# Optimization experiments

Hardware: AMD Instinct MI355X
Metric: run time of the kernel (lower is better)

## Reference

```python
import jax, jax.numpy as jnp
import numpy as np

NNZ = 4_194_304
IN_FEATURES = 4096
OUT_FEATURES = 4096
BATCH = 4
SEQ = 2048


def setup_inputs() -> dict:
    key = jax.random.key(0)
    k1, k2, k3, k4, k5, k6 = jax.random.split(key, 6)
    x = jax.random.normal(k1, (BATCH, SEQ, IN_FEATURES), dtype=jnp.float32)
    rows = jax.random.randint(k2, (NNZ,), 0, OUT_FEATURES, dtype=jnp.int32)
    cols = jax.random.randint(k3, (NNZ,), 0, IN_FEATURES, dtype=jnp.int32)
    w_real = jax.random.normal(k4, (NNZ,), dtype=jnp.float32)
    w_imag = jax.random.normal(k5, (NNZ,), dtype=jnp.float32)
    phase_angles = jax.random.uniform(k6, (BATCH,), dtype=jnp.float32) * 2.0 * np.pi
    return {
        "x": x,
        "rows": rows,
        "cols": cols,
        "w_real": w_real,
        "w_imag": w_imag,
        "phase_angles": phase_angles,
        "out_features": OUT_FEATURES,
    }


def reference(x, rows, cols, w_real, w_imag, phase_angles, out_features):
    B, S, F_in = x.shape
    N = B * S
    x_flat = x.reshape(N, F_in)  # [N, F_in]
    # per-flattened-row cosine phase (phase is per-batch, repeated over seq)
    cos_p = jnp.cos(jnp.repeat(phase_angles, S))  # [N]
    # assemble sparse COO weights into dense (out, in) matrices (duplicates sum)
    Wr = jnp.zeros((out_features, F_in), dtype=x_flat.dtype).at[rows, cols].add(w_real)
    Wi = jnp.zeros((out_features, F_in), dtype=x_flat.dtype).at[rows, cols].add(w_imag)
    # out[n, r] = sum_e x[n, cols[e]] * (w_real[e] + cos(phase[n]) * w_imag[e])
    out = x_flat @ Wr.T + cos_p[:, None] * (x_flat @ Wi.T)  # [N, out]
    return out.reshape(B, S, out_features)
```

## Files before the change

### kernel.cpp

```cpp
#include <hip/hip_runtime.h>


#define K_IN   4096
#define F_OUT  4096
#define SEQ    2048
#define NROW   8192
#define NNZ    4194304
#define WELEM  16777216
#define NBUCK  1024
#define SEGB   5120

typedef float  f32x4  __attribute__((ext_vector_type(4)));
typedef __bf16 bf16x8 __attribute__((ext_vector_type(8)));
typedef unsigned short u16x8 __attribute__((ext_vector_type(8)));

__device__ __forceinline__ unsigned short f2bf(float f) {
  unsigned u = __builtin_bit_cast(unsigned, f);
  u += 0x7fffu + ((u >> 16) & 1u);
  return (unsigned short)(u >> 16);
}
__device__ __forceinline__ float bf2f(unsigned short b) {
  return __builtin_bit_cast(float, (unsigned)b << 16);
}

__global__ __launch_bounds__(1024) void bin_kernel(
    const int* __restrict__ rows, const int* __restrict__ cols,
    const float* __restrict__ wre, const float* __restrict__ wim,
    unsigned* __restrict__ cursor, unsigned long long* __restrict__ records,
    const float* __restrict__ x, unsigned short* __restrict__ Xb) {
  const int b = blockIdx.x;
  if (b < 256) {
    __shared__ unsigned cnt[NBUCK];
    const int tid = threadIdx.x;
    const int e0 = b << 14;
    cnt[tid] = 0u;
    __syncthreads();
    #pragma unroll
    for (int i = 0; i < 16; ++i)
      atomicAdd(&cnt[((unsigned)rows[e0 + (i << 10) + tid]) >> 2], 1u);
    __syncthreads();
    {
      const unsigned c = cnt[tid];
      unsigned base = 0u;
      if (c) base = atomicAdd(&cursor[tid], c);
      cnt[tid] = base;
    }
    __syncthreads();
    for (int i = 0; i < 16; ++i) {
      const int e = e0 + (i << 10) + tid;
      const unsigned r  = (unsigned)rows[e];
      const unsigned bk = r >> 2;
      const unsigned rank = atomicAdd(&cnt[bk], 1u);
      const unsigned pk = (unsigned)f2bf(wre[e]) | ((unsigned)f2bf(wim[e]) << 16);
      if (rank < SEGB)
        records[(size_t)bk * SEGB + rank] =
            ((unsigned long long)pk << 32) | ((r & 3u) << 12) | (unsigned)cols[e];
    }
  } else {
    const size_t i8 = (((size_t)(b - 256) << 10) + threadIdx.x) << 3;
    f32x4 a = *(const f32x4*)(x + i8);
    f32x4 c = *(const f32x4*)(x + i8 + 4);
    u16x8 v;
    v[0] = f2bf(a[0]); v[1] = f2bf(a[1]); v[2] = f2bf(a[2]); v[3] = f2bf(a[3]);
    v[4] = f2bf(c[0]); v[5] = f2bf(c[1]); v[6] = f2bf(c[2]); v[7] = f2bf(c[3]);
    *(u16x8*)(Xb + i8) = v;
  }
}

__global__ __launch_bounds__(512) void assemble_kernel(
    const unsigned* __restrict__ cursor,
    const unsigned long long* __restrict__ records,
    const float* __restrict__ phase, unsigned short* __restrict__ Wb) {
  __shared__ float accRe[16384];
  __shared__ float accIm[16384];
  const int bk  = blockIdx.x;
  const int tid = threadIdx.x;
  #pragma unroll
  for (int i = 0; i < 32; ++i) {
    accRe[(i << 9) + tid] = 0.f;
    accIm[(i << 9) + tid] = 0.f;
  }
  __syncthreads();
  unsigned cnt = cursor[bk];
  if (cnt > SEGB) cnt = SEGB;
  const unsigned long long* seg = records + (size_t)bk * SEGB;
  for (unsigned i = tid; i < cnt; i += 512) {
    const unsigned long long rec = seg[i];
    const unsigned s = (unsigned)rec & 16383u;
    atomicAdd(&accRe[s], bf2f((unsigned short)((rec >> 32) & 0xffffu)));
    atomicAdd(&accIm[s], bf2f((unsigned short)(rec >> 48)));
  }
  __syncthreads();
  float cb[4];
  cb[0] = cosf(phase[0]); cb[1] = cosf(phase[1]);
  cb[2] = cosf(phase[2]); cb[3] = cosf(phase[3]);
  #pragma unroll
  for (int it = 0; it < 32; ++it) {
    const int s = (it << 9) + tid;
    const float re = accRe[s];
    const float im = accIm[s];
    #pragma unroll
    for (int bb = 0; bb < 4; ++bb)
      Wb[((size_t)bb << 24) + ((size_t)bk << 14) + s] = f2bf(re + cb[bb] * im);
  }
}

#define GLOAD_LDS(g, l)                                                        \
  __builtin_amdgcn_global_load_lds(                                            \
      (const __attribute__((address_space(1))) unsigned int*)(g),              \
      (__attribute__((address_space(3))) unsigned int*)(l), 16, 0, 0)

__global__ __launch_bounds__(512, 2) void gemm_kernel(
    const unsigned short* __restrict__ Xb,
    const unsigned short* __restrict__ Wb,
    float* __restrict__ out) {
  __shared__ unsigned short lds[65536];

  const int tid  = threadIdx.x;
  const int wid  = tid >> 6;
  const int lane = tid & 63;
  const int wr   = wid >> 2;
  const int wc   = wid & 3;

  const int bid  = blockIdx.x;
  const int swz  = ((bid & 7) << 6) | (bid >> 3);
  const int brow = swz >> 4;
  const int bcol = swz & 15;
  const size_t M0 = (size_t)brow << 8;
  const int batch = brow >> 3;
  const unsigned short* Ap = Xb + M0 * K_IN;
  const unsigned short* Bp = Wb + ((size_t)batch << 24) + (((size_t)bcol << 8) * K_IN);

  const int srow = lane >> 3;
  const int gsl  = ((lane & 7) ^ srow) << 3;
  const int lrow = lane & 15;
  const int lr7  = lane & 7;
  const int sb   = lane >> 4;

  f32x4 acc[8][4] = {};

#define STAGE(buf, k0)                                                         \
  {                                                                            \
    _Pragma("unroll")                                                          \
    for (int l = 0; l < 4; ++l) {                                              \
      const int rr = (l << 6) + (wid << 3);                                    \
      GLOAD_LDS(Ap + (size_t)(rr + srow) * K_IN + (size_t)((k0) + gsl),        \
                &lds[((buf) << 15) + (rr << 6)]);                              \
    }                                                                          \
    _Pragma("unroll")                                                          \
    for (int l = 0; l < 4; ++l) {                                              \
      const int rr = (l << 6) + (wid << 3);                                    \
      GLOAD_LDS(Bp + (size_t)(rr + srow) * K_IN + (size_t)((k0) + gsl),        \
                &lds[((buf) << 15) + 16384 + (rr << 6)]);                      \
    }                                                                          \
  }

#define COMPUTE(buf)                                                           \
  {                                                                            \
    const unsigned short* la = &lds[(buf) << 15];                              \
    const unsigned short* lb = &lds[((buf) << 15) + 16384];                    \
    _Pragma("unroll")                                                          \
    for (int t = 0; t < 2; ++t) {                                              \
      const int cs = (((t << 2) + sb) ^ lr7) << 3;                             \
      bf16x8 af[8], bff[4];                                                    \
      _Pragma("unroll")                                                        \
      for (int m = 0; m < 8; ++m)                                              \
        af[m] = *(const bf16x8*)&la[(((wr << 7) + (m << 4) + lrow) << 6) + cs];\
      _Pragma("unroll")                                                        \
      for (int n = 0; n < 4; ++n)                                              \
        bff[n] = *(const bf16x8*)&lb[(((wc << 6) + (n << 4) + lrow) << 6) + cs];\
      __builtin_amdgcn_s_setprio(1);                                           \
      _Pragma("unroll")                                                        \
      for (int m = 0; m < 8; ++m)                                              \
        _Pragma("unroll")                                                      \
        for (int n = 0; n < 4; ++n)                                            \
          acc[m][n] = __builtin_amdgcn_mfma_f32_16x16x32_bf16(                 \
              af[m], bff[n], acc[m][n], 0, 0, 0);                              \
      __builtin_amdgcn_s_setprio(0);                                           \
    }                                                                          \
  }

  STAGE(0, 0);
  int cur = 0;
  for (int t = 0; t < 63; ++t) {
    STAGE(cur ^ 1, (t + 1) << 6);
    asm volatile("s_waitcnt vmcnt(8)\n\ts_barrier" ::: "memory");
    COMPUTE(cur);
    asm volatile("s_barrier" ::: "memory");
    cur ^= 1;
  }
  asm volatile("s_waitcnt vmcnt(0)\n\ts_barrier" ::: "memory");
  COMPUTE(cur);

  const int ch = lane >> 4;
  float* op = out + (M0 + (size_t)(wr << 7)) * F_OUT + ((size_t)bcol << 8) + (wc << 6);
  #pragma unroll
  for (int m = 0; m < 8; ++m)
    #pragma unroll
    for (int n = 0; n < 4; ++n)
      #pragma unroll
      for (int j = 0; j < 4; ++j)
        op[(size_t)((m << 4) + (ch << 2) + j) * F_OUT + (n << 4) + lrow] = acc[m][n][j];
#undef STAGE
#undef COMPUTE
}

__global__ __launch_bounds__(256) void scatter_kernel(
    const int* __restrict__ rows, const int* __restrict__ cols,
    const float* __restrict__ wre, const float* __restrict__ wim,
    unsigned short* __restrict__ Wcb) {
  int e = blockIdx.x * 256 + threadIdx.x;
  int r = rows[e];
  int c = cols[e];
  unsigned pk = (unsigned)f2bf(wre[e]) | ((unsigned)f2bf(wim[e]) << 16);
  size_t idx = ((size_t)r << 12) + (size_t)c;
  asm volatile("global_atomic_pk_add_bf16 %0, %1, off"
               :: "v"(Wcb + (idx << 1)), "v"(pk) : "memory");
}
__global__ __launch_bounds__(256) void fold_kernel(
    const unsigned short* __restrict__ Wcb, const float* __restrict__ phase,
    unsigned short* __restrict__ Wb) {
  size_t i8 = ((size_t)blockIdx.x * 256 + threadIdx.x) << 3;
  float cb[4];
  cb[0] = cosf(phase[0]); cb[1] = cosf(phase[1]);
  cb[2] = cosf(phase[2]); cb[3] = cosf(phase[3]);
  const unsigned short* p = Wcb + (i8 << 1);
  u16x8 a = *(const u16x8*)(p);
  u16x8 b = *(const u16x8*)(p + 8);
  float rr[8], ii[8];
  rr[0] = bf2f(a[0]); ii[0] = bf2f(a[1]);
  rr[1] = bf2f(a[2]); ii[1] = bf2f(a[3]);
  rr[2] = bf2f(a[4]); ii[2] = bf2f(a[5]);
  rr[3] = bf2f(a[6]); ii[3] = bf2f(a[7]);
  rr[4] = bf2f(b[0]); ii[4] = bf2f(b[1]);
  rr[5] = bf2f(b[2]); ii[5] = bf2f(b[3]);
  rr[6] = bf2f(b[4]); ii[6] = bf2f(b[5]);
  rr[7] = bf2f(b[6]); ii[7] = bf2f(b[7]);
  #pragma unroll
  for (int bb = 0; bb < 4; ++bb) {
    float c = cb[bb];
    u16x8 v;
    #pragma unroll
    for (int j = 0; j < 8; ++j) v[j] = f2bf(rr[j] + c * ii[j]);
    *(u16x8*)(Wb + ((size_t)bb << 24) + i8) = v;
  }
}
__global__ __launch_bounds__(256) void xconv_kernel(
    const float* __restrict__ x, unsigned short* __restrict__ Xb) {
  size_t i8 = ((size_t)blockIdx.x * 256 + threadIdx.x) << 3;
  f32x4 a = *(const f32x4*)(x + i8);
  f32x4 c = *(const f32x4*)(x + i8 + 4);
  u16x8 v;
  v[0] = f2bf(a[0]); v[1] = f2bf(a[1]); v[2] = f2bf(a[2]); v[3] = f2bf(a[3]);
  v[4] = f2bf(c[0]); v[5] = f2bf(c[1]); v[6] = f2bf(c[2]); v[7] = f2bf(c[3]);
  *(u16x8*)(Xb + i8) = v;
}
__global__ __launch_bounds__(256) void naive_kernel(
    const float* __restrict__ x, const unsigned short* __restrict__ Wcb,
    const float* __restrict__ phase, float* __restrict__ out) {
  int n = blockIdx.x >> 4;
  int r = ((blockIdx.x & 15) << 8) | threadIdx.x;
  float cb = cosf(phase[n >> 11]);
  const float* xp = x + ((size_t)n << 12);
  const unsigned short* wc = Wcb + (((size_t)r << 12) << 1);
  float ar = 0.f, ai = 0.f;
  for (int k = 0; k < K_IN; ++k) {
    float xv = xp[k];
    ar += xv * bf2f(wc[2 * k]);
    ai += xv * bf2f(wc[2 * k + 1]);
  }
  out[((size_t)n << 12) + r] = ar + cb * ai;
}

extern "C" void kernel_launch(void* const* d_in, const int* in_sizes, int n_in,
                              void* d_out, int out_size, void* d_ws, size_t ws_size,
                              hipStream_t stream) {
  const float* x     = (const float*)d_in[0];
  const int*   rows  = (const int*)d_in[1];
  const int*   cols  = (const int*)d_in[2];
  const float* wre   = (const float*)d_in[3];
  const float* wim   = (const float*)d_in[4];
  const float* phase = (const float*)d_in[5];
  float* out = (float*)d_out;

  const size_t WS_FULL = (size_t)268435456;
  const size_t WS_MAIN = (size_t)201326592;
  if (ws_size >= WS_FULL) {
    unsigned short*     Wb      = (unsigned short*)d_ws;
    unsigned short*     Xb      = (unsigned short*)((char*)d_ws + (size_t)134217728);
    unsigned long long* records = (unsigned long long*)((char*)d_ws + (size_t)201326592);
    unsigned*           cursor  = (unsigned*)((char*)d_ws + (size_t)251658240);
    hipMemsetAsync(cursor, 0, NBUCK * sizeof(unsigned), stream);
    bin_kernel<<<256 + 4096, 1024, 0, stream>>>(rows, cols, wre, wim,
                                                cursor, records, x, Xb);
    assemble_kernel<<<NBUCK, 512, 0, stream>>>(cursor, records, phase, Wb);
    gemm_kernel<<<512, 512, 0, stream>>>(Xb, Wb, out);
  } else if (ws_size >= WS_MAIN) {
    unsigned short* Wcb = (unsigned short*)d_ws;
    unsigned short* Wb  = (unsigned short*)((char*)d_ws + (size_t)67108864);
    unsigned short* Xb  = (unsigned short*)d_ws;
    hipMemsetAsync(d_ws, 0, (size_t)WELEM * 4, stream);
    scatter_kernel<<<NNZ / 256, 256, 0, stream>>>(rows, cols, wre, wim, Wcb);
    fold_kernel<<<WELEM / 8 / 256, 256, 0, stream>>>(Wcb, phase, Wb);
    xconv_kernel<<<(size_t)NROW * K_IN / 8 / 256, 256, 0, stream>>>(x, Xb);
    gemm_kernel<<<512, 512, 0, stream>>>(Xb, Wb, out);
  } else {
    unsigned short* Wcb = (unsigned short*)d_ws;
    hipMemsetAsync(d_ws, 0, (size_t)WELEM * 4, stream);
    scatter_kernel<<<NNZ / 256, 256, 0, stream>>>(rows, cols, wre, wim, Wcb);
    naive_kernel<<<NROW * 16, 256, 0, stream>>>(x, Wcb, phase, out);
  }
}
```

Baseline: 458.6 us.

## Interleave half-tile global loads with quadrant MFMA phases in GEMM main loop

Replaces the double-buffered stage/compute loop with a finer-grained schedule. Each 64-wide K tile is split into four MFMA quadrants, and half-tile A/B global-to-LDS loads and LDS fragment reads are interleaved between them under explicit barriers and waitcnts. The goal is to overlap memory traffic with matrix-core work more evenly and to cut the register pressure from holding all fragments at once. The cost is many more barriers per iteration and a hand-tuned ordering that is fragile to get right.

```diff
diff --git a/kernel.cpp b/kernel.cpp
--- a/kernel.cpp
+++ b/kernel.cpp
@@ -136,61 +136,90 @@
   const int lrow = lane & 15;
   const int lr7  = lane & 7;
   const int sb   = lane >> 4;
+  const int cs0 = (sb ^ lr7) << 3;
+  const int cs1 = ((4 + sb) ^ lr7) << 3;
 
   f32x4 acc[8][4] = {};
-
-#define STAGE(buf, k0)                                                         \
+  bf16x8 af[8], bf0[4], bf1[4];
+
+#define STA_H(buf, h, k0)                                                      \
   {                                                                            \
     _Pragma("unroll")                                                          \
-    for (int l = 0; l < 4; ++l) {                                              \
-      const int rr = (l << 6) + (wid << 3);                                    \
-      GLOAD_LDS(Ap + (size_t)(rr + srow) * K_IN + (size_t)((k0) + gsl),        \
-                &lds[((buf) << 15) + (rr << 6)]);                              \
+    for (int ll = 0; ll < 2; ++ll) {                                           \
+      const int rb = (((ll << 1) + (h)) << 6) + (wid << 3);                    \
+      GLOAD_LDS(Ap + (size_t)(rb + srow) * K_IN + (size_t)((k0) + gsl),        \
+                &lds[((buf) << 15) + (rb << 6)]);                              \
     }                                                                          \
+  }
+#define STB_H(buf, h, k0)                                                      \
+  {                                                                            \
     _Pragma("unroll")                                                          \
-    for (int l = 0; l < 4; ++l) {                                              \
-      const int rr = (l << 6) + (wid << 3);                                    \
-      GLOAD_LDS(Bp + (size_t)(rr + srow) * K_IN + (size_t)((k0) + gsl),        \
-                &lds[((buf) << 15) + 16384 + (rr << 6)]);                      \
+    for (int j = 0; j < 2; ++j) {                                              \
+      const int rb = (((j << 1) + (wid >> 2)) << 6) + ((h) << 5) + ((wid & 3) << 3); \
+      GLOAD_LDS(Bp + (size_t)(rb + srow) * K_IN + (size_t)((k0) + gsl),        \
+                &lds[((buf) << 15) + 16384 + (rb << 6)]);                      \
     }                                                                          \
   }
-
-#define COMPUTE(buf)                                                           \
-  {                                                                            \
-    const unsigned short* la = &lds[(buf) << 15];                              \
-    const unsigned short* lb = &lds[((buf) << 15) + 16384];                    \
+#define DS_A(buf, mbase)                                                       \
+  _Pragma("unroll")                                                            \
+  for (int m = 0; m < 4; ++m) {                                                \
+    const int ro = ((buf) << 15) + (((wr << 7) + (((mbase) + m) << 4) + lrow) << 6); \
+    af[m]     = *(const bf16x8*)&lds[ro + cs0];                                \
+    af[m + 4] = *(const bf16x8*)&lds[ro + cs1];                                \
+  }
+#define DS_B(buf, nbase, arr)                                                  \
+  _Pragma("unroll")                                                            \
+  for (int n = 0; n < 2; ++n) {                                                \
+    const int ro = ((buf) << 15) + 16384 + (((wc << 6) + (((nbase) + n) << 4) + lrow) << 6); \
+    arr[n]     = *(const bf16x8*)&lds[ro + cs0];                               \
+    arr[n + 2] = *(const bf16x8*)&lds[ro + cs1];                               \
+  }
+#define MM(MB, NB, arr)                                                        \
+  __builtin_amdgcn_s_setprio(1);                                               \
+  _Pragma("unroll")                                                            \
+  for (int m = 0; m < 4; ++m)                                                  \
     _Pragma("unroll")                                                          \
-    for (int t = 0; t < 2; ++t) {                                              \
-      const int cs = (((t << 2) + sb) ^ lr7) << 3;                             \
-      bf16x8 af[8], bff[4];                                                    \
-      _Pragma("unroll")                                                        \
-      for (int m = 0; m < 8; ++m)                                              \
-        af[m] = *(const bf16x8*)&la[(((wr << 7) + (m << 4) + lrow) << 6) + cs];\
-      _Pragma("unroll")                                                        \
-      for (int n = 0; n < 4; ++n)                                              \
-        bff[n] = *(const bf16x8*)&lb[(((wc << 6) + (n << 4) + lrow) << 6) + cs];\
-      __builtin_amdgcn_s_setprio(1);                                           \
-      _Pragma("unroll")                                                        \
-      for (int m = 0; m < 8; ++m)                                              \
-        _Pragma("unroll")                                                      \
-        for (int n = 0; n < 4; ++n)                                            \
-          acc[m][n] = __builtin_amdgcn_mfma_f32_16x16x32_bf16(                 \
-              af[m], bff[n], acc[m][n], 0, 0, 0);                              \
-      __builtin_amdgcn_s_setprio(0);                                           \
+    for (int n = 0; n < 2; ++n) {                                              \
+      acc[(MB) + m][(NB) + n] = __builtin_amdgcn_mfma_f32_16x16x32_bf16(       \
+          af[m], arr[n], acc[(MB) + m][(NB) + n], 0, 0, 0);                    \
+      acc[(MB) + m][(NB) + n] = __builtin_amdgcn_mfma_f32_16x16x32_bf16(       \
+          af[m + 4], arr[n + 2], acc[(MB) + m][(NB) + n], 0, 0, 0);            \
     }                                                                          \
-  }
-
-  STAGE(0, 0);
-  int cur = 0;
-  for (int t = 0; t < 63; ++t) {
-    STAGE(cur ^ 1, (t + 1) << 6);
-    asm volatile("s_waitcnt vmcnt(8)\n\ts_barrier" ::: "memory");
-    COMPUTE(cur);
-    asm volatile("s_barrier" ::: "memory");
-    cur ^= 1;
-  }
-  asm volatile("s_waitcnt vmcnt(0)\n\ts_barrier" ::: "memory");
-  COMPUTE(cur);
+  __builtin_amdgcn_s_setprio(0)
+#define BARR __builtin_amdgcn_s_barrier()
+#define LGKM0 do { asm volatile("s_waitcnt lgkmcnt(0)" ::: "memory");          \
+                   __builtin_amdgcn_sched_barrier(0); } while (0)
+#define VMC(n) asm volatile("s_waitcnt vmcnt(" #n ")" ::: "memory")
+
+  STA_H(0, 0, 0); STB_H(0, 0, 0); STB_H(0, 1, 0); STA_H(0, 1, 0);
+  STA_H(1, 0, 64); STB_H(1, 0, 64);
+  VMC(4);
+  BARR;
+
+  for (int I = 0; I < 31; ++I) {
+    const int k1 = (2 * I + 1) << 6;
+    const int k2 = (2 * I + 2) << 6;
+    const int k3 = (2 * I + 3) << 6;
+    DS_A(0, 0); DS_B(0, 0, bf0); STB_H(1, 1, k1); BARR; LGKM0; MM(0, 0, bf0); BARR;
+    DS_B(0, 2, bf1);             STA_H(1, 1, k1); BARR; LGKM0; MM(0, 2, bf1); BARR;
+    DS_A(0, 4);                  STA_H(0, 0, k2); BARR; LGKM0; MM(4, 0, bf0); BARR;
+    STB_H(0, 0, k2); VMC(4);                      BARR;        MM(4, 2, bf1); BARR;
+    DS_A(1, 0); DS_B(1, 0, bf0); STB_H(0, 1, k2); BARR; LGKM0; MM(0, 0, bf0); BARR;
+    DS_B(1, 2, bf1);             STA_H(0, 1, k2); BARR; LGKM0; MM(0, 2, bf1); BARR;
+    DS_A(1, 4);                  STA_H(1, 0, k3); BARR; LGKM0; MM(4, 0, bf0); BARR;
+    STB_H(1, 0, k3); VMC(4);                      BARR;        MM(4, 2, bf1); BARR;
+  }
+  {
+    const int k1 = 63 << 6;
+    DS_A(0, 0); DS_B(0, 0, bf0); STB_H(1, 1, k1); BARR; LGKM0; MM(0, 0, bf0); BARR;
+    DS_B(0, 2, bf1);             STA_H(1, 1, k1); BARR; LGKM0; MM(0, 2, bf1); BARR;
+    DS_A(0, 4);                                   BARR; LGKM0; MM(4, 0, bf0); BARR;
+    VMC(0);                                       BARR;        MM(4, 2, bf1); BARR;
+    DS_A(1, 0); DS_B(1, 0, bf0);                  BARR; LGKM0; MM(0, 0, bf0); BARR;
+    DS_B(1, 2, bf1);                              BARR; LGKM0; MM(0, 2, bf1); BARR;
+    DS_A(1, 4);                                   BARR; LGKM0; MM(4, 0, bf0); BARR;
+    MM(4, 2, bf1);
+  }
 
   const int ch = lane >> 4;
   float* op = out + (M0 + (size_t)(wr << 7)) * F_OUT + ((size_t)bcol << 8) + (wc << 6);
@@ -201,8 +230,14 @@
       #pragma unroll
       for (int j = 0; j < 4; ++j)
         op[(size_t)((m << 4) + (ch << 2) + j) * F_OUT + (n << 4) + lrow] = acc[m][n][j];
-#undef STAGE
-#undef COMPUTE
+#undef STA_H
+#undef STB_H
+#undef DS_A
+#undef DS_B
+#undef MM
+#undef BARR
+#undef LGKM0
+#undef VMC
 }
 
 __global__ __launch_bounds__(256) void scatter_kernel(
```

Result: slower. 554.3 us (+20.9%).
